# Performance work log

Measured on AMD Instinct MI355X. Metric: run time of the kernel, lower is better.

Reference implementation:

```python
import jax, jax.numpy as jnp
import numpy as np

NUM_EMBEDDINGS = 4096
EMBEDDING_DIM = 512
N_TOKENS = 32768
COMMITMENT_COST = 0.25


def setup_inputs() -> dict:
    key = jax.random.key(0)
    k1, k2 = jax.random.split(key)
    flat_input = jax.random.normal(k1, (N_TOKENS, EMBEDDING_DIM), dtype=jnp.float32)
    # torch init: uniform(-1/K, 1/K)
    weight = jax.random.uniform(k2, (NUM_EMBEDDINGS, EMBEDDING_DIM), dtype=jnp.float32,
                                minval=-1.0 / NUM_EMBEDDINGS, maxval=1.0 / NUM_EMBEDDINGS)
    return {"flat_input": flat_input, "weight": weight}


def reference(flat_input, weight):
    distances = (jnp.sum(flat_input ** 2, axis=1, keepdims=True)
                 + jnp.sum(weight ** 2, axis=1)
                 - 2.0 * jnp.matmul(flat_input, weight.T))
    encoding_indices = jnp.argmin(distances, axis=1)  # [N]
    # one-hot @ weight == direct gather of codebook rows
    quantized = weight[encoding_indices]  # [N, D]

    e_latent_loss = jnp.mean((jax.lax.stop_gradient(quantized) - flat_input) ** 2, axis=1)
    q_latent_loss = jnp.mean((quantized - jax.lax.stop_gradient(flat_input)) ** 2, axis=1)
    loss = q_latent_loss + COMMITMENT_COST * e_latent_loss  # [N]

    # straight-through estimator
    quantized_st = flat_input + jax.lax.stop_gradient(quantized - flat_input)

    # avg_probs = mean of one-hot encodings over batch = normalized code counts
    counts = jnp.zeros((NUM_EMBEDDINGS,), dtype=flat_input.dtype).at[encoding_indices].add(1.0)
    avg_probs = counts / flat_input.shape[0]
    perplexity = jnp.exp(-jnp.sum(avg_probs * jnp.log(avg_probs + 1e-10)))

    return quantized_st, loss, perplexity, encoding_indices
```

## Files before the change

### kernel.cpp

```cpp
#include <hip/hip_runtime.h>
#include <math.h>

#define N_TOK 32768
#define K_CODES 4096
#define DIM 512
#define COMMIT 0.25f
#define NCAND 8
#define NSPLIT 2
#define SPLIT_CODES (K_CODES / NSPLIT)
#define NITER (SPLIT_CODES / 128)
#define BIAS 0.125f

typedef short s16x8 __attribute__((ext_vector_type(8)));
typedef float f32x4 __attribute__((ext_vector_type(4)));
typedef unsigned int uint32;
typedef unsigned long long u64;
typedef unsigned short u16;

__device__ __forceinline__ u16 f2bf(float f) {
    uint32 b = __float_as_uint(f);
    return (u16)((b + 0x7FFFu + ((b >> 16) & 1u)) >> 16);
}

__device__ __forceinline__ void gload16(const u16* g, u16* l) {
    __builtin_amdgcn_global_load_lds(
        (const __attribute__((address_space(1))) void*)g,
        (__attribute__((address_space(3))) void*)l,
        16, 0, 0);
}

__global__ __launch_bounds__(256) void tobf16_kernel(const float* __restrict__ src,
                                                     u16* __restrict__ dst, int n4) {
    int i = blockIdx.x * 256 + threadIdx.x;
    int stride = gridDim.x * 256;
    for (; i < n4; i += stride) {
        float4 v = ((const float4*)src)[i];
        ushort4 o;
        o.x = f2bf(v.x); o.y = f2bf(v.y); o.z = f2bf(v.z); o.w = f2bf(v.w);
        ((ushort4*)dst)[i] = o;
    }
}

__global__ __launch_bounds__(256) void rowsq_np_kernel(const float* __restrict__ a,
                                                       float* __restrict__ out,
                                                       int nrows) {
    #pragma clang fp contract(off)
    const int gw   = (blockIdx.x * 256 + threadIdx.x) >> 6;
    const int lane = threadIdx.x & 63;
    const int row  = gw * 8 + (lane >> 3);
    const int j    = lane & 7;
    if (row >= nrows) return;
    const float* p = a + (size_t)row * DIM;
    float blk[4];
    #pragma unroll
    for (int b = 0; b < 4; ++b) {
        const float* q = p + b * 128;
        float v = q[j];
        float r = v * v;
        for (int i = 8; i < 128; i += 8) { float u = q[i + j]; r += u * u; }
        float s1 = r  + __shfl_xor(r, 1);
        float s2 = s1 + __shfl_xor(s1, 2);
        float s3 = s2 + __shfl_xor(s2, 4);
        blk[b] = s3;
    }
    float res = (blk[0] + blk[1]) + (blk[2] + blk[3]);
    if (j == 0) out[row] = res;
}

__global__ __launch_bounds__(512, 2) void screen_kernel(const u16* __restrict__ xb,
                                                        const u16* __restrict__ wb,
                                                        const float* __restrict__ w2f,
                                                        u64* __restrict__ candPart) {
    __shared__ __attribute__((aligned(16))) u16 POOL[32768];

    const int tid  = threadIdx.x;
    const int wv   = tid >> 6;
    const int wt   = wv >> 2;
    const int wc   = wv & 3;
    const int lane = tid & 63;
    const int quad = lane >> 4;
    const int n15  = lane & 15;
    const int m0   = blockIdx.x * 128;
    const int sbase = blockIdx.y * SPLIT_CODES;

    const int l8  = lane >> 3;
    const int qsw = (lane & 7) ^ l8;

    const u16* xg0 = xb + (size_t)(m0 + wv * 16 + l8) * DIM + qsw * 8;
    const u16* xg1 = xg0 + (size_t)8 * DIM;
    const u16* wit = wb + (size_t)(sbase + wv * 16 + l8) * DIM + qsw * 8;

    uint32 r1[16], r2[16];
    #pragma unroll
    for (int i = 0; i < 16; ++i) { r1[i] = 0xFFFFFFFFu; r2[i] = 0xFFFFFFFFu; }

    {
        u16* lx = &POOL[wv * 1024];
        u16* lw = &POOL[16384 + wv * 1024];
        gload16(xg0, lx);
        gload16(xg1, lx + 512);
        gload16(wit, lw);
        gload16(wit + (size_t)8 * DIM, lw + 512);
    }
    __syncthreads();

    for (int it = 0; it < NITER; ++it) {
        const int nbase = sbase + it * 128;

        float w2pb[2];
        #pragma unroll
        for (int c = 0; c < 2; ++c) w2pb[c] = w2f[nbase + wc * 32 + c * 16 + n15] + BIAS;

        f32x4 acc[4][2];
        #pragma unroll
        for (int i = 0; i < 4; ++i)
            #pragma unroll
            for (int c = 0; c < 2; ++c) acc[i][c] = (f32x4){0.f, 0.f, 0.f, 0.f};

        for (int kc = 0; kc < 8; ++kc) {
            if (kc < 7) {
                const int nb = (kc + 1) & 1;
                const int ko = (kc + 1) * 64;
                u16* lx = &POOL[nb * 8192 + wv * 1024];
                u16* lw = &POOL[16384 + nb * 8192 + wv * 1024];
                gload16(xg0 + ko, lx);
                gload16(xg1 + ko, lx + 512);
                gload16(wit + ko, lw);
                gload16(wit + (size_t)8 * DIM + ko, lw + 512);
            } else if (it < NITER - 1) {
                const u16* wn = wit + (size_t)128 * DIM;
                u16* lx = &POOL[wv * 1024];
                u16* lw = &POOL[16384 + wv * 1024];
                gload16(xg0, lx);
                gload16(xg1, lx + 512);
                gload16(wn, lw);
                gload16(wn + (size_t)8 * DIM, lw + 512);
            }

            const u16* X = &POOL[(kc & 1) * 8192];
            const u16* W = &POOL[16384 + (kc & 1) * 8192];
            #pragma unroll
            for (int s = 0; s < 2; ++s) {
                const int lq = s * 4 + quad;
                s16x8 af[4], bf[2];
                #pragma unroll
                for (int i = 0; i < 4; ++i) {
                    const int tr = wt * 64 + i * 16 + n15;
                    af[i] = *(const s16x8*)&X[tr * 64 + (lq ^ (tr & 7)) * 8];
                }
                #pragma unroll
                for (int c = 0; c < 2; ++c) {
                    const int cr = wc * 32 + c * 16 + n15;
                    bf[c] = *(const s16x8*)&W[cr * 64 + (lq ^ (cr & 7)) * 8];
                }
                #pragma unroll
                for (int i = 0; i < 4; ++i)
                    #pragma unroll
                    for (int c = 0; c < 2; ++c)
                        acc[i][c] = __builtin_amdgcn_mfma_f32_16x16x32_bf16(af[i], bf[c], acc[i][c], 0, 0, 0);
            }
            __syncthreads();
        }

        #pragma unroll
        for (int i = 0; i < 4; ++i)
            #pragma unroll
            for (int r = 0; r < 4; ++r) {
                const int ti = i * 4 + r;
                #pragma unroll
                for (int c = 0; c < 2; ++c) {
                    float s = fmaf(-2.0f, acc[i][c][r], w2pb[c]);
                    uint32 key = (__float_as_uint(s) & 0xFFFFFFC0u) | (uint32)((it << 1) | c);
                    uint32 mx = r1[ti] > key ? r1[ti] : key;
                    r1[ti] = r1[ti] < key ? r1[ti] : key;
                    r2[ti] = r2[ti] < mx ? r2[ti] : mx;
                }
            }
        wit += (size_t)128 * DIM;
    }

    u64* MS = (u64*)POOL;
    for (int phase = 0; phase < 2; ++phase) {
        __syncthreads();
        if (wt == phase) {
            #pragma unroll
            for (int ti = 0; ti < 16; ++ti) {
                const int i = ti >> 2, r = ti & 3;
                const int tloc = i * 16 + quad * 4 + r;
                #pragma unroll
                for (int e = 0; e < 2; ++e) {
                    uint32 k  = e ? r2[ti] : r1[ti];
                    uint32 vb = k & 0xFFFFFFC0u;
                    uint32 id = k & 63u;
                    uint32 code = (uint32)(sbase + (id >> 1) * 128 + wc * 32 + (id & 1) * 16 + n15);
                    MS[tloc * 128 + (wc * 16 + n15) * 2 + e] = ((u64)vb << 32) | code;
                }
            }
        }
        __syncthreads();
        if (tid < 64) {
            u64 best[6];
            #pragma unroll
            for (int c = 0; c < 6; ++c) best[c] = 0xFFFFFFFFFFFFFFFFull;
            for (int e = 0; e < 128; ++e) {
                u64 v = MS[tid * 128 + e];
                if (v < best[5]) {
                    best[5] = v;
                    #pragma unroll
                    for (int p = 5; p > 0; --p)
                        if (best[p] < best[p - 1]) { u64 tv = best[p]; best[p] = best[p - 1]; best[p - 1] = tv; }
                }
            }
            const int token = m0 + phase * 64 + tid;
            u64* dst = candPart + ((size_t)blockIdx.y * N_TOK + token) * 6;
            #pragma unroll
            for (int c = 0; c < 6; ++c) dst[c] = best[c];
        }
    }
}

__global__ __launch_bounds__(256) void mergecand_kernel(const u64* __restrict__ candPart,
                                                        int* __restrict__ candF) {
    int t = blockIdx.x * 256 + threadIdx.x;
    u64 best[NCAND];
    #pragma unroll
    for (int c = 0; c < NCAND; ++c) best[c] = 0xFFFFFFFFFFFFFFFFull;
    for (int s = 0; s < NSPLIT; ++s) {
        const u64* src = candPart + ((size_t)s * N_TOK + t) * 6;
        #pragma unroll
        for (int c = 0; c < 6; ++c) {
            u64 v = src[c];
            if (v < best[NCAND - 1]) {
                best[NCAND - 1] = v;
                #pragma unroll
                for (int p = NCAND - 1; p > 0; --p)
                    if (best[p] < best[p - 1]) { u64 tv = best[p]; best[p] = best[p - 1]; best[p - 1] = tv; }
            }
        }
    }
    #pragma unroll
    for (int c = 0; c < NCAND; ++c) candF[(size_t)t * NCAND + c] = (int)(best[c] & 0xFFFu);
}

__global__ __launch_bounds__(256) void refine_kernel(const float* __restrict__ x,
                                                     const float* __restrict__ w,
                                                     const float* __restrict__ x2np,
                                                     const float* __restrict__ w2np,
                                                     const int* __restrict__ cand,
                                                     int* __restrict__ idx) {
    const int t    = blockIdx.x * 4 + (threadIdx.x >> 6);
    const int lane = threadIdx.x & 63;

    const float* xr = x + (size_t)t * DIM;
    float xv[8];
    #pragma unroll
    for (int j = 0; j < 8; ++j) xv[j] = xr[lane + 64 * j];
    const float x2 = x2np[t];

    float bd = 3.4e38f;
    int   bk = 0x7fffffff;
    for (int c = 0; c < NCAND; ++c) {
        int k = cand[(size_t)t * NCAND + c];
        const float* wr = w + (size_t)k * DIM;
        double m = 0.0;
        #pragma unroll
        for (int j = 0; j < 8; ++j)
            m = fma((double)xv[j], (double)wr[lane + 64 * j], m);
        #pragma unroll
        for (int off = 32; off >= 1; off >>= 1) m += __shfl_down(m, off);
        if (lane == 0) {
            #pragma clang fp contract(off)
            float m32 = (float)m;
            float T1  = x2 + w2np[k];
            float d   = T1 - 2.0f * m32;
            if (d < bd || (d == bd && k < bk)) { bd = d; bk = k; }
        }
    }
    if (lane == 0) idx[t] = bk;
}

__global__ __launch_bounds__(256) void gather_kernel(const float* __restrict__ x,
                                                     const float* __restrict__ w,
                                                     const int* __restrict__ idx,
                                                     float* __restrict__ out_q,
                                                     float* __restrict__ out_loss,
                                                     float* __restrict__ out_ind,
                                                     int* __restrict__ counts) {
    const int wave = threadIdx.x >> 6;
    const int lane = threadIdx.x & 63;
    const int token = blockIdx.x * 4 + wave;
    const int k = idx[token];

    const float4* xr = (const float4*)(x + (size_t)token * DIM);
    const float4* wr = (const float4*)(w + (size_t)k * DIM);
    float4*       qo = (float4*)(out_q + (size_t)token * DIM);

    float ss = 0.f;
    #pragma unroll
    for (int j = 0; j < 2; ++j) {
        int e = lane + j * 64;
        float4 xv = xr[e];
        float4 wv = wr[e];
        float4 d, o;
        d.x = wv.x - xv.x; o.x = xv.x + d.x;
        d.y = wv.y - xv.y; o.y = xv.y + d.y;
        d.z = wv.z - xv.z; o.z = xv.z + d.z;
        d.w = wv.w - xv.w; o.w = xv.w + d.w;
        ss += d.x * d.x + d.y * d.y + d.z * d.z + d.w * d.w;
        qo[e] = o;
    }
    #pragma unroll
    for (int off = 32; off >= 1; off >>= 1) ss += __shfl_down(ss, off);
    if (lane == 0) {
        float lm = ss * (1.0f / DIM);
        out_loss[token] = lm + COMMIT * lm;
        out_ind[token] = (float)k;
        atomicAdd(&counts[k], 1);
    }
}

__global__ __launch_bounds__(256) void perplex_kernel(const int* __restrict__ counts,
                                                      float* __restrict__ out2) {
    __shared__ double red[4];
    const int tid = threadIdx.x;
    const int lane = tid & 63;
    const int wid = tid >> 6;
    double s = 0.0;
    for (int t = tid; t < K_CODES; t += 256) {
        int c = counts[t];
        if (c) {
            double p = (double)c * (1.0 / N_TOK);
            s += p * log(p + 1e-10);
        }
    }
    #pragma unroll
    for (int off = 32; off >= 1; off >>= 1) s += __shfl_down(s, off);
    if (lane == 0) red[wid] = s;
    __syncthreads();
    if (tid == 0) {
        double t = red[0] + red[1] + red[2] + red[3];
        out2[0] = (float)exp(-t);
    }
}

extern "C" void kernel_launch(void* const* d_in, const int* in_sizes, int n_in,
                              void* d_out, int out_size, void* d_ws, size_t ws_size,
                              hipStream_t stream) {
    const float* x = (const float*)d_in[0];
    const float* w = (const float*)d_in[1];

    float* out0 = (float*)d_out;
    float* out1 = out0 + (size_t)N_TOK * DIM;
    float* out2 = out1 + N_TOK;
    float* out3 = out2 + 1;

    u64*   candPart = (u64*)d_ws;
    float* x2np     = (float*)(candPart + (size_t)NSPLIT * N_TOK * 6);
    float* w2np     = x2np + N_TOK;
    int*   idx      = (int*)(w2np + K_CODES);
    int*   counts   = idx + N_TOK;
    int*   candF    = counts + K_CODES;
    u16*   x_bf     = (u16*)(candF + (size_t)N_TOK * NCAND);
    u16*   w_bf     = x_bf + (size_t)N_TOK * DIM;

    hipMemsetAsync(counts, 0, K_CODES * sizeof(int), stream);

    tobf16_kernel<<<4096, 256, 0, stream>>>(x, x_bf, N_TOK * DIM / 4);
    tobf16_kernel<<<2048, 256, 0, stream>>>(w, w_bf, K_CODES * DIM / 4);
    rowsq_np_kernel<<<N_TOK / 32, 256, 0, stream>>>(x, x2np, N_TOK);
    rowsq_np_kernel<<<K_CODES / 32, 256, 0, stream>>>(w, w2np, K_CODES);
    screen_kernel<<<dim3(N_TOK / 128, NSPLIT), 512, 0, stream>>>(x_bf, w_bf, w2np, candPart);
    mergecand_kernel<<<N_TOK / 256, 256, 0, stream>>>(candPart, candF);
    refine_kernel<<<N_TOK / 4, 256, 0, stream>>>(x, w, x2np, w2np, candF, idx);
    gather_kernel<<<N_TOK / 4, 256, 0, stream>>>(x, w, idx, out0, out1, out3, counts);
    perplex_kernel<<<1, 256, 0, stream>>>(counts, out2);
}
```

Before: 471.4 us.

## Enlarge screen kernel tile to 256x256 with wider per-wave code strips

```diff
diff --git a/kernel.cpp b/kernel.cpp
--- a/kernel.cpp
+++ b/kernel.cpp
@@ -8,7 +8,7 @@
 #define NCAND 8
 #define NSPLIT 2
 #define SPLIT_CODES (K_CODES / NSPLIT)
-#define NITER (SPLIT_CODES / 128)
+#define NITER (SPLIT_CODES / 256)
 #define BIAS 0.125f
 
 typedef short s16x8 __attribute__((ext_vector_type(8)));
@@ -71,93 +71,87 @@
                                                         const u16* __restrict__ wb,
                                                         const float* __restrict__ w2f,
                                                         u64* __restrict__ candPart) {
-    __shared__ __attribute__((aligned(16))) u16 POOL[32768];
+    __shared__ __attribute__((aligned(16))) u16 POOL[65536];
 
     const int tid  = threadIdx.x;
     const int wv   = tid >> 6;
-    const int wt   = wv >> 2;
-    const int wc   = wv & 3;
+    const int wt   = wv >> 1;
+    const int wcc  = wv & 1;
     const int lane = tid & 63;
     const int quad = lane >> 4;
     const int n15  = lane & 15;
-    const int m0   = blockIdx.x * 128;
+    const int m0   = blockIdx.x * 256;
     const int sbase = blockIdx.y * SPLIT_CODES;
 
     const int l8  = lane >> 3;
     const int qsw = (lane & 7) ^ l8;
 
-    const u16* xg0 = xb + (size_t)(m0 + wv * 16 + l8) * DIM + qsw * 8;
-    const u16* xg1 = xg0 + (size_t)8 * DIM;
-    const u16* wit = wb + (size_t)(sbase + wv * 16 + l8) * DIM + qsw * 8;
+    const u16* xg = xb + (size_t)(m0 + wv * 32 + l8) * DIM + qsw * 8;
+    const u16* wit = wb + (size_t)(sbase + wv * 32 + l8) * DIM + qsw * 8;
 
     uint32 r1[16], r2[16];
     #pragma unroll
     for (int i = 0; i < 16; ++i) { r1[i] = 0xFFFFFFFFu; r2[i] = 0xFFFFFFFFu; }
 
-    {
-        u16* lx = &POOL[wv * 1024];
-        u16* lw = &POOL[16384 + wv * 1024];
-        gload16(xg0, lx);
-        gload16(xg1, lx + 512);
-        gload16(wit, lw);
-        gload16(wit + (size_t)8 * DIM, lw + 512);
+    #pragma unroll
+    for (int j = 0; j < 4; ++j) {
+        gload16(xg + (size_t)(j * 8) * DIM, &POOL[wv * 2048 + j * 512]);
+        gload16(wit + (size_t)(j * 8) * DIM, &POOL[32768 + wv * 2048 + j * 512]);
     }
     __syncthreads();
 
     for (int it = 0; it < NITER; ++it) {
-        const int nbase = sbase + it * 128;
-
-        float w2pb[2];
-        #pragma unroll
-        for (int c = 0; c < 2; ++c) w2pb[c] = w2f[nbase + wc * 32 + c * 16 + n15] + BIAS;
-
-        f32x4 acc[4][2];
+        const int nbase = sbase + it * 256;
+
+        float w2pb[8];
+        #pragma unroll
+        for (int c = 0; c < 8; ++c) w2pb[c] = w2f[nbase + wcc * 128 + c * 16 + n15] + BIAS;
+
+        f32x4 acc[4][8];
         #pragma unroll
         for (int i = 0; i < 4; ++i)
             #pragma unroll
-            for (int c = 0; c < 2; ++c) acc[i][c] = (f32x4){0.f, 0.f, 0.f, 0.f};
+            for (int c = 0; c < 8; ++c) acc[i][c] = (f32x4){0.f, 0.f, 0.f, 0.f};
 
         for (int kc = 0; kc < 8; ++kc) {
             if (kc < 7) {
                 const int nb = (kc + 1) & 1;
                 const int ko = (kc + 1) * 64;
-                u16* lx = &POOL[nb * 8192 + wv * 1024];
-                u16* lw = &POOL[16384 + nb * 8192 + wv * 1024];
-                gload16(xg0 + ko, lx);
-                gload16(xg1 + ko, lx + 512);
-                gload16(wit + ko, lw);
-                gload16(wit + (size_t)8 * DIM + ko, lw + 512);
+                #pragma unroll
+                for (int j = 0; j < 4; ++j) {
+                    gload16(xg + (size_t)(j * 8) * DIM + ko,
+                            &POOL[nb * 16384 + wv * 2048 + j * 512]);
+                    gload16(wit + (size_t)(j * 8) * DIM + ko,
+                            &POOL[32768 + nb * 16384 + wv * 2048 + j * 512]);
+                }
             } else if (it < NITER - 1) {
-                const u16* wn = wit + (size_t)128 * DIM;
-                u16* lx = &POOL[wv * 1024];
-                u16* lw = &POOL[16384 + wv * 1024];
-                gload16(xg0, lx);
-                gload16(xg1, lx + 512);
-                gload16(wn, lw);
-                gload16(wn + (size_t)8 * DIM, lw + 512);
-            }
-
-            const u16* X = &POOL[(kc & 1) * 8192];
-            const u16* W = &POOL[16384 + (kc & 1) * 8192];
+                const u16* wn = wit + (size_t)256 * DIM;
+                #pragma unroll
+                for (int j = 0; j < 4; ++j) {
+                    gload16(xg + (size_t)(j * 8) * DIM, &POOL[wv * 2048 + j * 512]);
+                    gload16(wn + (size_t)(j * 8) * DIM, &POOL[32768 + wv * 2048 + j * 512]);
+                }
+            }
+
+            const u16* X = &POOL[(kc & 1) * 16384];
+            const u16* W = &POOL[32768 + (kc & 1) * 16384];
             #pragma unroll
             for (int s = 0; s < 2; ++s) {
-                const int lq = s * 4 + quad;
-                s16x8 af[4], bf[2];
+                const int qoff = ((s * 4 + quad) ^ (n15 & 7)) * 8;
+                s16x8 af[4];
                 #pragma unroll
                 for (int i = 0; i < 4; ++i) {
                     const int tr = wt * 64 + i * 16 + n15;
-                    af[i] = *(const s16x8*)&X[tr * 64 + (lq ^ (tr & 7)) * 8];
-                }
-                #pragma unroll
-                for (int c = 0; c < 2; ++c) {
-                    const int cr = wc * 32 + c * 16 + n15;
-                    bf[c] = *(const s16x8*)&W[cr * 64 + (lq ^ (cr & 7)) * 8];
-                }
-                #pragma unroll
-                for (int i = 0; i < 4; ++i)
+                    af[i] = *(const s16x8*)&X[tr * 64 + qoff];
+                }
+                #pragma unroll
+                for (int c = 0; c < 8; ++c) {
+                    const int cr = wcc * 128 + c * 16 + n15;
+                    s16x8 bf = *(const s16x8*)&W[cr * 64 + qoff];
                     #pragma unroll
-                    for (int c = 0; c < 2; ++c)
-                        acc[i][c] = __builtin_amdgcn_mfma_f32_16x16x32_bf16(af[i], bf[c], acc[i][c], 0, 0, 0);
+                    for (int i = 0; i < 4; ++i)
+                        acc[i][c] = __builtin_amdgcn_mfma_f32_16x16x32_bf16(af[i], bf, acc[i][c], 0, 0, 0);
+                }
             }
             __syncthreads();
         }
@@ -168,54 +162,49 @@
             for (int r = 0; r < 4; ++r) {
                 const int ti = i * 4 + r;
                 #pragma unroll
-                for (int c = 0; c < 2; ++c) {
+                for (int c = 0; c < 8; ++c) {
                     float s = fmaf(-2.0f, acc[i][c][r], w2pb[c]);
-                    uint32 key = (__float_as_uint(s) & 0xFFFFFFC0u) | (uint32)((it << 1) | c);
+                    uint32 key = (__float_as_uint(s) & 0xFFFFFFC0u) | (uint32)((it << 3) | c);
                     uint32 mx = r1[ti] > key ? r1[ti] : key;
                     r1[ti] = r1[ti] < key ? r1[ti] : key;
                     r2[ti] = r2[ti] < mx ? r2[ti] : mx;
                 }
             }
-        wit += (size_t)128 * DIM;
+        wit += (size_t)256 * DIM;
     }
 
     u64* MS = (u64*)POOL;
-    for (int phase = 0; phase < 2; ++phase) {
-        __syncthreads();
-        if (wt == phase) {
-            #pragma unroll
-            for (int ti = 0; ti < 16; ++ti) {
-                const int i = ti >> 2, r = ti & 3;
-                const int tloc = i * 16 + quad * 4 + r;
-                #pragma unroll
-                for (int e = 0; e < 2; ++e) {
-                    uint32 k  = e ? r2[ti] : r1[ti];
-                    uint32 vb = k & 0xFFFFFFC0u;
-                    uint32 id = k & 63u;
-                    uint32 code = (uint32)(sbase + (id >> 1) * 128 + wc * 32 + (id & 1) * 16 + n15);
-                    MS[tloc * 128 + (wc * 16 + n15) * 2 + e] = ((u64)vb << 32) | code;
-                }
-            }
-        }
-        __syncthreads();
-        if (tid < 64) {
-            u64 best[6];
-            #pragma unroll
-            for (int c = 0; c < 6; ++c) best[c] = 0xFFFFFFFFFFFFFFFFull;
-            for (int e = 0; e < 128; ++e) {
-                u64 v = MS[tid * 128 + e];
-                if (v < best[5]) {
-                    best[5] = v;
-                    #pragma unroll
-                    for (int p = 5; p > 0; --p)
-                        if (best[p] < best[p - 1]) { u64 tv = best[p]; best[p] = best[p - 1]; best[p - 1] = tv; }
-                }
-            }
-            const int token = m0 + phase * 64 + tid;
-            u64* dst = candPart + ((size_t)blockIdx.y * N_TOK + token) * 6;
-            #pragma unroll
-            for (int c = 0; c < 6; ++c) dst[c] = best[c];
-        }
+    #pragma unroll
+    for (int ti = 0; ti < 16; ++ti) {
+        const int i = ti >> 2, r = ti & 3;
+        const int tloc = wt * 64 + i * 16 + quad * 4 + r;
+        #pragma unroll
+        for (int e = 0; e < 2; ++e) {
+            uint32 k  = e ? r2[ti] : r1[ti];
+            uint32 vb = k & 0xFFFFFFC0u;
+            uint32 id = k & 63u;
+            uint32 code = (uint32)(sbase + (id >> 3) * 256 + wcc * 128 + (id & 7) * 16 + n15);
+            MS[tloc * 64 + (wcc * 16 + n15) * 2 + e] = ((u64)vb << 32) | code;
+        }
+    }
+    __syncthreads();
+    if (tid < 256) {
+        u64 best[6];
+        #pragma unroll
+        for (int c = 0; c < 6; ++c) best[c] = 0xFFFFFFFFFFFFFFFFull;
+        for (int e = 0; e < 64; ++e) {
+            u64 v = MS[tid * 64 + e];
+            if (v < best[5]) {
+                best[5] = v;
+                #pragma unroll
+                for (int p = 5; p > 0; --p)
+                    if (best[p] < best[p - 1]) { u64 tv = best[p]; best[p] = best[p - 1]; best[p - 1] = tv; }
+            }
+        }
+        const int token = m0 + tid;
+        u64* dst = candPart + ((size_t)blockIdx.y * N_TOK + token) * 6;
+        #pragma unroll
+        for (int c = 0; c < 6; ++c) dst[c] = best[c];
     }
 }
 
@@ -369,7 +358,7 @@
     tobf16_kernel<<<2048, 256, 0, stream>>>(w, w_bf, K_CODES * DIM / 4);
     rowsq_np_kernel<<<N_TOK / 32, 256, 0, stream>>>(x, x2np, N_TOK);
     rowsq_np_kernel<<<K_CODES / 32, 256, 0, stream>>>(w, w2np, K_CODES);
-    screen_kernel<<<dim3(N_TOK / 128, NSPLIT), 512, 0, stream>>>(x_bf, w_bf, w2np, candPart);
+    screen_kernel<<<dim3(N_TOK / 256, NSPLIT), 512, 0, stream>>>(x_bf, w_bf, w2np, candPart);
     mergecand_kernel<<<N_TOK / 256, 256, 0, stream>>>(candPart, candF);
     refine_kernel<<<N_TOK / 4, 256, 0, stream>>>(x, w, x2np, w2np, candF, idx);
     gather_kernel<<<N_TOK / 4, 256, 0, stream>>>(x, w, idx, out0, out1, out3, counts);
```

After: 510.3 us. 1.08x slower.
